# Performance work log

Hardware: AMD Instinct MI355X
Metric: run time of the kernel (lower is better)

The kernel has to match this reference:

```python
import jax, jax.numpy as jnp
import numpy as np

EPS = 1e-5

def layernorm(x, g, b):
    mu = jnp.mean(x, axis=-1, keepdims=True)
    var = jnp.var(x, axis=-1, keepdims=True)
    return (x - mu) / jnp.sqrt(var + EPS) * g + b

def hpmlp(x, wa, ba, wb, bb):
    # Linear(in,H) -> GELU(erf) -> Linear(H,H); dropout is identity in eval
    h = jax.nn.gelu(x @ wa + ba, approximate=False)
    return h @ wb + bb

def setup_inputs() -> dict:
    key = jax.random.key(0)
    ks = jax.random.split(key, 8)
    B, S, H = 16, 4096, 768
    s = 0.02
    return {
        "tokens": jax.random.normal(ks[0], (B, S + 1, H), jnp.float32),
        "lengths": jax.random.randint(ks[1], (B,), 1, S + 1),
        "q": jax.random.normal(ks[2], (2, H), jnp.float32) * s,
        "ln_g": jnp.ones((H,), jnp.float32),
        "ln_b": jnp.zeros((H,), jnp.float32),
        "w1a": jax.random.normal(ks[3], (3 * H, H), jnp.float32) * s,
        "b1a": jnp.zeros((H,), jnp.float32),
        "w1b": jax.random.normal(ks[4], (H, H), jnp.float32) * s,
        "b1b": jnp.zeros((H,), jnp.float32),
        "w2a": jax.random.normal(ks[5], (3 * H, H), jnp.float32) * s,
        "b2a": jnp.zeros((H,), jnp.float32),
        "w2b": jax.random.normal(ks[6], (H, H), jnp.float32) * s,
        "b2b": jnp.zeros((H,), jnp.float32),
    }

def reference(tokens, lengths, q, ln_g, ln_b, w1a, b1a, w1b, b1b, w2a, b2a, w2b, b2b):
    clf = tokens[:, 0]          # [B, H]
    x = tokens[:, 1:]           # [B, S, H]
    B, S, H = x.shape
    mask = jnp.arange(S)[None, :] < lengths[:, None]      # [B, S]
    m3 = mask[..., None]
    denom = lengths.astype(x.dtype)[:, None]
    mean_pooled = jnp.sum(jnp.where(m3, x, 0.0), axis=1) / denom
    max_pooled = jnp.max(jnp.where(m3, x, -jnp.inf), axis=1)
    min_pooled = jnp.min(jnp.where(m3, x, jnp.inf), axis=1)
    # PatchMerger with 2 learned queries over length-masked tokens
    xn = layernorm(x, ln_g, ln_b)                          # [B, S, H]
    logits = jnp.einsum("qh,bsh->bqs", q, xn) * (H ** -0.5)
    logits = jnp.where(mask[:, None, :], logits, -jnp.inf)
    attn = jax.nn.softmax(logits, axis=-1)                 # [B, 2, S]
    pmp = jnp.einsum("bqs,bsh->bqh", attn, xn)             # [B, 2, H]
    pooled_trad = jnp.concatenate([mean_pooled, max_pooled, min_pooled], -1)  # [B, 3H]
    pooled_learn = jnp.concatenate([pmp.reshape(B, 2 * H), clf], -1)          # [B, 3H]
    return jnp.concatenate([
        hpmlp(pooled_trad, w1a, b1a, w1b, b1b),
        hpmlp(pooled_learn, w2a, b2a, w2b, b2b),
    ], -1)
```

## Files before the change

### kernel.cpp

```cpp
#include <hip/hip_runtime.h>
#include <cmath>
#include <cstddef>

#define HD    768
#define BATCH 16
#define SROW  4097
#define NCH   64
#define CS    64
#define TPW   16
#define REC   3856
#define NK1   36
#define NK2   12
#define QSCALE 0.03608439182435161f

__device__ inline void wred4(float& a, float& b, float& c, float& d) {
#pragma unroll
  for (int off = 32; off > 0; off >>= 1) {
    a += __shfl_xor(a, off, 64);
    b += __shfl_xor(b, off, 64);
    c += __shfl_xor(c, off, 64);
    d += __shfl_xor(d, off, 64);
  }
}

__global__ __launch_bounds__(256, 3) void k1_pass(
    const float* __restrict__ tokens, const int* __restrict__ lengths,
    const float* __restrict__ q, const float* __restrict__ ln_g,
    const float* __restrict__ ln_b, float* __restrict__ rec)
{
  const int b = blockIdx.y, c = blockIdx.x;
  const int tid = threadIdx.x, w = tid >> 6, lane = tid & 63;
  const int len = lengths[b];
  if (c * CS >= len) return;

  float gq0[12], gq1[12];
  float G0 = 0.f, G1 = 0.f, C0 = 0.f, C1 = 0.f;
#pragma unroll
  for (int e = 0; e < 3; ++e) {
    const int off = e * 256 + lane * 4;
    const float4 qa = *(const float4*)(q + off);
    const float4 qb = *(const float4*)(q + HD + off);
    const float4 gg = *(const float4*)(ln_g + off);
    const float4 bb = *(const float4*)(ln_b + off);
    const float qav[4] = {qa.x, qa.y, qa.z, qa.w};
    const float qbv[4] = {qb.x, qb.y, qb.z, qb.w};
    const float ggv[4] = {gg.x, gg.y, gg.z, gg.w};
    const float bbv[4] = {bb.x, bb.y, bb.z, bb.w};
#pragma unroll
    for (int j = 0; j < 4; ++j) {
      const float g0 = ggv[j] * qav[j] * QSCALE;
      const float g1 = ggv[j] * qbv[j] * QSCALE;
      gq0[e * 4 + j] = g0;  gq1[e * 4 + j] = g1;
      G0 += g0;  G1 += g1;
      C0 = fmaf(bbv[j] * QSCALE, qav[j], C0);
      C1 = fmaf(bbv[j] * QSCALE, qbv[j], C1);
    }
  }
  wred4(G0, G1, C0, C1);

  float psum[12], pmax[12], pmin[12], A0[12], A1[12];
#pragma unroll
  for (int i = 0; i < 12; ++i) {
    psum[i] = 0.f; pmax[i] = -INFINITY; pmin[i] = INFINITY;
    A0[i] = 0.f; A1[i] = 0.f;
  }
  float m0 = -INFINITY, l0 = 0.f, B0 = 0.f;
  float m1 = -INFINITY, l1 = 0.f, B1 = 0.f;

  const float* xr0 = tokens + ((size_t)b * SROW + 1 + c * CS + w * TPW) * HD
                   + lane * 4;
  const int sbase = c * CS + w * TPW;

  for (int t = 0; t < TPW; ++t) {
    if (sbase + t >= len) break;
    const float* xr = xr0 + (size_t)t * HD;
    float xv[12];
#pragma unroll
    for (int e = 0; e < 3; ++e)
      *(float4*)(xv + 4 * e) = *(const float4*)(xr + e * 256);

    float s1 = 0.f, s2 = 0.f, dx0 = 0.f, dx1 = 0.f;
#pragma unroll
    for (int i = 0; i < 12; ++i) {
      s1 += xv[i];
      s2 = fmaf(xv[i], xv[i], s2);
      dx0 = fmaf(xv[i], gq0[i], dx0);
      dx1 = fmaf(xv[i], gq1[i], dx1);
    }
    wred4(s1, s2, dx0, dx1);
    const float mu   = s1 * (1.f / HD);
    const float var  = fmaf(-mu, mu, s2 * (1.f / HD));
    const float rstd = rsqrtf(var + 1e-5f);
    const float d0 = fmaf(rstd, fmaf(-mu, G0, dx0), C0);
    const float d1 = fmaf(rstd, fmaf(-mu, G1, dx1), C1);

    const float mn0 = fmaxf(m0, d0);
    const float al0 = __expf(m0 - mn0);
    const float p0  = __expf(d0 - mn0);
    const float c0  = p0 * rstd;
    l0 = fmaf(l0, al0, p0);  B0 = fmaf(B0, al0, c0 * mu);  m0 = mn0;

    const float mn1 = fmaxf(m1, d1);
    const float al1 = __expf(m1 - mn1);
    const float p1  = __expf(d1 - mn1);
    const float c1  = p1 * rstd;
    l1 = fmaf(l1, al1, p1);  B1 = fmaf(B1, al1, c1 * mu);  m1 = mn1;

#pragma unroll
    for (int i = 0; i < 12; ++i) {
      psum[i] += xv[i];
      pmax[i] = fmaxf(pmax[i], xv[i]);
      pmin[i] = fminf(pmin[i], xv[i]);
      A0[i] = fmaf(A0[i], al0, c0 * xv[i]);
      A1[i] = fmaf(A1[i], al1, c1 * xv[i]);
    }
  }

  __shared__ float ls[4][2][HD];
  __shared__ float lml[4][6];
#pragma unroll
  for (int e = 0; e < 3; ++e) {
    const int off = e * 256 + lane * 4;
    *(float4*)&ls[w][0][off] = *(const float4*)(psum + 4 * e);
    *(float4*)&ls[w][1][off] = *(const float4*)(pmax + 4 * e);
  }
  if (lane == 0) {
    lml[w][0] = m0; lml[w][1] = l0; lml[w][2] = B0;
    lml[w][3] = m1; lml[w][4] = l1; lml[w][5] = B1;
  }
  __syncthreads();

  float bm0 = -INFINITY, bm1 = -INFINITY;
#pragma unroll
  for (int wv = 0; wv < 4; ++wv) {
    bm0 = fmaxf(bm0, lml[wv][0]);
    bm1 = fmaxf(bm1, lml[wv][3]);
  }
  float sc0[4], sc1[4], bl0 = 0.f, bB0 = 0.f, bl1 = 0.f, bB1 = 0.f;
#pragma unroll
  for (int wv = 0; wv < 4; ++wv) {
    sc0[wv] = (lml[wv][1] > 0.f) ? __expf(lml[wv][0] - bm0) : 0.f;
    sc1[wv] = (lml[wv][4] > 0.f) ? __expf(lml[wv][3] - bm1) : 0.f;
    bl0 = fmaf(lml[wv][1], sc0[wv], bl0);  bB0 = fmaf(lml[wv][2], sc0[wv], bB0);
    bl1 = fmaf(lml[wv][4], sc1[wv], bl1);  bB1 = fmaf(lml[wv][5], sc1[wv], bB1);
  }

  float* r = rec + (size_t)(b * NCH + c) * REC;
#pragma unroll
  for (int e = 0; e < 3; ++e) {
    const int h = tid + 256 * e;
    float su = 0.f, mx = -INFINITY;
#pragma unroll
    for (int wv = 0; wv < 4; ++wv) {
      su += ls[wv][0][h];
      mx = fmaxf(mx, ls[wv][1][h]);
    }
    r[h] = su;  r[HD + h] = mx;
  }
  __syncthreads();
#pragma unroll
  for (int e = 0; e < 3; ++e) {
    const int off = e * 256 + lane * 4;
    *(float4*)&ls[w][0][off] = *(const float4*)(pmin + 4 * e);
    *(float4*)&ls[w][1][off] = *(const float4*)(A0 + 4 * e);
  }
  __syncthreads();
#pragma unroll
  for (int e = 0; e < 3; ++e) {
    const int h = tid + 256 * e;
    float mn_ = INFINITY, a0 = 0.f;
#pragma unroll
    for (int wv = 0; wv < 4; ++wv) {
      mn_ = fminf(mn_, ls[wv][0][h]);
      a0 = fmaf(ls[wv][1][h], sc0[wv], a0);
    }
    r[2 * HD + h] = mn_;  r[3 * HD + h] = a0;
  }
  __syncthreads();
#pragma unroll
  for (int e = 0; e < 3; ++e) {
    const int off = e * 256 + lane * 4;
    *(float4*)&ls[w][0][off] = *(const float4*)(A1 + 4 * e);
  }
  __syncthreads();
#pragma unroll
  for (int e = 0; e < 3; ++e) {
    const int h = tid + 256 * e;
    float a1 = 0.f;
#pragma unroll
    for (int wv = 0; wv < 4; ++wv) a1 = fmaf(ls[wv][0][h], sc1[wv], a1);
    r[4 * HD + h] = a1;
  }
  if (tid == 0) {
    r[3840] = bm0; r[3841] = bl0; r[3842] = bB0;
    r[3843] = bm1; r[3844] = bl1; r[3845] = bB1;
  }
}

__global__ __launch_bounds__(256) void k2_combine(
    const float* __restrict__ rec, const float* __restrict__ tokens,
    const int* __restrict__ lengths, const float* __restrict__ ln_g,
    const float* __restrict__ ln_b, const float* __restrict__ b1b,
    const float* __restrict__ b2b, float* __restrict__ pt,
    float* __restrict__ pl, float* __restrict__ out)
{
  const int b = blockIdx.y, seg = blockIdx.x;
  const int tid = threadIdx.x, ln = tid & 63, cs = tid >> 6;
  const int h = seg * 64 + ln;
  const int len = lengths[b];
  const int nch = (len + CS - 1) / CS;
  const float* rb = rec + (size_t)b * NCH * REC;

  float mg0 = -INFINITY, mg1 = -INFINITY;
  for (int c = 0; c < nch; ++c) {
    const float* rm = rb + (size_t)c * REC + 3840;
    mg0 = fmaxf(mg0, rm[0]);
    mg1 = fmaxf(mg1, rm[3]);
  }
  float lg0 = 0.f, Bg0 = 0.f, lg1 = 0.f, Bg1 = 0.f;
  for (int c = 0; c < nch; ++c) {
    const float* rm = rb + (size_t)c * REC + 3840;
    const float e0 = __expf(rm[0] - mg0);
    const float e1 = __expf(rm[3] - mg1);
    lg0 = fmaf(rm[1], e0, lg0);  Bg0 = fmaf(rm[2], e0, Bg0);
    lg1 = fmaf(rm[4], e1, lg1);  Bg1 = fmaf(rm[5], e1, Bg1);
  }

  float S = 0.f, MX = -INFINITY, MN = INFINITY, A0 = 0.f, A1 = 0.f;
  for (int cc = 0; cc < NCH / 4; ++cc) {
    const int c = cs * (NCH / 4) + cc;
    if (c >= nch) break;
    const float* r = rb + (size_t)c * REC;
    const float e0 = __expf(r[3840] - mg0);
    const float e1 = __expf(r[3843] - mg1);
    S += r[h];
    MX = fmaxf(MX, r[HD + h]);
    MN = fminf(MN, r[2 * HD + h]);
    A0 = fmaf(r[3 * HD + h], e0, A0);
    A1 = fmaf(r[4 * HD + h], e1, A1);
  }

  __shared__ float lbuf[5][4][64];
  lbuf[0][cs][ln] = S;  lbuf[1][cs][ln] = MX; lbuf[2][cs][ln] = MN;
  lbuf[3][cs][ln] = A0; lbuf[4][cs][ln] = A1;
  __syncthreads();
  if (cs == 0) {
#pragma unroll
    for (int k = 1; k < 4; ++k) {
      S  += lbuf[0][k][ln];
      MX  = fmaxf(MX, lbuf[1][k][ln]);
      MN  = fminf(MN, lbuf[2][k][ln]);
      A0 += lbuf[3][k][ln];
      A1 += lbuf[4][k][ln];
    }
    const float invlen = 1.f / (float)len;
    const float il0 = 1.f / lg0, il1 = 1.f / lg1;
    const float gg = ln_g[h], bb = ln_b[h];
    float* ptb = pt + (size_t)b * 2304;
    float* plb = pl + (size_t)b * 2304;
    ptb[h] = S * invlen;
    ptb[HD + h] = MX;
    ptb[2 * HD + h] = MN;
    plb[h]      = fmaf(gg, (A0 - Bg0) * il0, bb);
    plb[HD + h] = fmaf(gg, (A1 - Bg1) * il1, bb);
    plb[2 * HD + h] = tokens[(size_t)b * SROW * HD + h];
  }

  const int gidx = (b * 12 + seg) * 256 + tid;
  if (gidx < 2 * BATCH * HD) {
    const int j = gidx % HD, r2 = (gidx / HD) % 2;
    out[gidx] = (r2 ? b2b : b1b)[j];
  }
}

__global__ __launch_bounds__(256) void k3_gemm1(
    const float* __restrict__ pt, const float* __restrict__ pl,
    const float* __restrict__ w1a, const float* __restrict__ w2a,
    float* __restrict__ part1)
{
  const int kseg = blockIdx.x, jseg = blockIdx.y, mlp = blockIdx.z;
  const int j = jseg * 256 + threadIdx.x;
  const float* xs = mlp ? pl : pt;
  const float* wA = mlp ? w2a : w1a;
  float acc[16];
#pragma unroll
  for (int bb = 0; bb < 16; ++bb) acc[bb] = 0.f;
  const int k0 = kseg * 64;
  for (int kk = 0; kk < 64; ++kk) {
    const int k = k0 + kk;
    const float wv = wA[(size_t)k * HD + j];
#pragma unroll
    for (int bb = 0; bb < 16; ++bb)
      acc[bb] = fmaf(xs[bb * 2304 + k], wv, acc[bb]);
  }
  float* p = part1 + (size_t)(kseg * 2 + mlp) * 16 * HD;
#pragma unroll
  for (int bb = 0; bb < 16; ++bb) p[bb * HD + j] = acc[bb];
}

__global__ __launch_bounds__(256) void k4_gemm2(
    const float* __restrict__ part1, const float* __restrict__ b1a,
    const float* __restrict__ b2a, const float* __restrict__ w1b,
    const float* __restrict__ w2b, float* __restrict__ out)
{
  const int kseg = blockIdx.x, jseg = blockIdx.y, mlp = blockIdx.z;
  const int tid = threadIdx.x;
  const int j = jseg * 256 + tid;
  const int k0 = kseg * 64;
  __shared__ float hs[16][64];

  const float* ba = mlp ? b2a : b1a;
#pragma unroll
  for (int u = 0; u < 4; ++u) {
    const int lin = tid + 256 * u;
    const int bb = lin >> 6, kk = lin & 63;
    const int k = k0 + kk;
    float acc = ba[k];
    for (int ks = 0; ks < NK1; ++ks)
      acc += part1[(size_t)((ks * 2 + mlp) * 16 + bb) * HD + k];
    hs[bb][kk] = 0.5f * acc * (1.f + erff(acc * 0.70710678118654752f));
  }
  __syncthreads();

  const float* wB = mlp ? w2b : w1b;
  float acc2[16];
#pragma unroll
  for (int bb = 0; bb < 16; ++bb) acc2[bb] = 0.f;
  for (int kk = 0; kk < 64; ++kk) {
    const float wv = wB[(size_t)(k0 + kk) * HD + j];
#pragma unroll
    for (int bb = 0; bb < 16; ++bb)
      acc2[bb] = fmaf(hs[bb][kk], wv, acc2[bb]);
  }
#pragma unroll
  for (int bb = 0; bb < 16; ++bb)
    unsafeAtomicAdd(&out[(size_t)bb * 1536 + mlp * HD + j], acc2[bb]);
}

extern "C" void kernel_launch(void* const* d_in, const int* in_sizes, int n_in,
                              void* d_out, int out_size, void* d_ws, size_t ws_size,
                              hipStream_t stream)
{
  const float* tokens = (const float*)d_in[0];
  const int*   lengths = (const int*)d_in[1];
  const float* q    = (const float*)d_in[2];
  const float* ln_g = (const float*)d_in[3];
  const float* ln_b = (const float*)d_in[4];
  const float* w1a  = (const float*)d_in[5];
  const float* b1a  = (const float*)d_in[6];
  const float* w1b  = (const float*)d_in[7];
  const float* b1b  = (const float*)d_in[8];
  const float* w2a  = (const float*)d_in[9];
  const float* b2a  = (const float*)d_in[10];
  const float* w2b  = (const float*)d_in[11];
  const float* b2b  = (const float*)d_in[12];
  float* out = (float*)d_out;

  float* ws    = (float*)d_ws;
  float* rec   = ws;
  float* pt    = rec + (size_t)BATCH * NCH * REC;
  float* pl    = pt + (size_t)BATCH * 2304;
  float* part1 = pl + (size_t)BATCH * 2304;

  hipLaunchKernelGGL(k1_pass, dim3(NCH, BATCH), dim3(256), 0, stream,
                     tokens, lengths, q, ln_g, ln_b, rec);
  hipLaunchKernelGGL(k2_combine, dim3(12, BATCH), dim3(256), 0, stream,
                     rec, tokens, lengths, ln_g, ln_b, b1b, b2b, pt, pl, out);
  hipLaunchKernelGGL(k3_gemm1, dim3(NK1, 3, 2), dim3(256), 0, stream,
                     pt, pl, w1a, w2a, part1);
  hipLaunchKernelGGL(k4_gemm2, dim3(NK2, 3, 2), dim3(256), 0, stream,
                     part1, b1a, b2a, w1b, w2b, out);
}
```

Measured before the change: 359.5 us.

## Prefetch next token row, parallelise softmax stats, atomically reduce GEMM1 partials

The token-streaming loop in k1 now software-prefetches the next row's three float4 loads before working on the current row, so load latency overlaps the reductions. k2 splits the per-chunk max and softmax-normaliser scans across four waves and initialises a hidden buffer with the first-layer biases. k3 halves its K-slice and accumulates into that buffer with atomics instead of writing 72 partial slabs, so k4 no longer sums partials before GELU. This adds atomic contention and register pressure in k1 in exchange for less serial work and less memory traffic.

```diff
diff --git a/kernel.cpp b/kernel.cpp
--- a/kernel.cpp
+++ b/kernel.cpp
@@ -9,8 +9,10 @@
 #define CS    64
 #define TPW   16
 #define REC   3856
-#define NK1   36
-#define NK2   12
+#define NK1   72
+#define K1SEG 32
+#define NK2   24
+#define K2SEG 32
 #define QSCALE 0.03608439182435161f
 
 __device__ inline void wred4(float& a, float& b, float& c, float& d) {
@@ -67,17 +69,30 @@
   float m0 = -INFINITY, l0 = 0.f, B0 = 0.f;
   float m1 = -INFINITY, l1 = 0.f, B1 = 0.f;
 
-  const float* xr0 = tokens + ((size_t)b * SROW + 1 + c * CS + w * TPW) * HD
-                   + lane * 4;
   const int sbase = c * CS + w * TPW;
-
-  for (int t = 0; t < TPW; ++t) {
-    if (sbase + t >= len) break;
-    const float* xr = xr0 + (size_t)t * HD;
+  const int rem0  = len - sbase;
+  const int nt    = rem0 < 0 ? 0 : (rem0 < TPW ? rem0 : TPW);
+
+  const float* xr = tokens + ((size_t)b * SROW + 1 + sbase) * HD + lane * 4;
+
+  float4 nxa, nxb, nxc;
+  if (nt > 0) {
+    nxa = *(const float4*)(xr);
+    nxb = *(const float4*)(xr + 256);
+    nxc = *(const float4*)(xr + 512);
+  }
+
+  for (int t = 0; t < nt; ++t) {
     float xv[12];
-#pragma unroll
-    for (int e = 0; e < 3; ++e)
-      *(float4*)(xv + 4 * e) = *(const float4*)(xr + e * 256);
+    *(float4*)(xv)     = nxa;
+    *(float4*)(xv + 4) = nxb;
+    *(float4*)(xv + 8) = nxc;
+    if (t + 1 < nt) {
+      xr += HD;
+      nxa = *(const float4*)(xr);
+      nxb = *(const float4*)(xr + 256);
+      nxc = *(const float4*)(xr + 512);
+    }
 
     float s1 = 0.f, s2 = 0.f, dx0 = 0.f, dx1 = 0.f;
 #pragma unroll
@@ -200,32 +215,39 @@
 __global__ __launch_bounds__(256) void k2_combine(
     const float* __restrict__ rec, const float* __restrict__ tokens,
     const int* __restrict__ lengths, const float* __restrict__ ln_g,
-    const float* __restrict__ ln_b, const float* __restrict__ b1b,
+    const float* __restrict__ ln_b, const float* __restrict__ b1a,
+    const float* __restrict__ b2a, const float* __restrict__ b1b,
     const float* __restrict__ b2b, float* __restrict__ pt,
-    float* __restrict__ pl, float* __restrict__ out)
+    float* __restrict__ pl, float* __restrict__ hbuf,
+    float* __restrict__ out)
 {
   const int b = blockIdx.y, seg = blockIdx.x;
   const int tid = threadIdx.x, ln = tid & 63, cs = tid >> 6;
-  const int h = seg * 64 + ln;
+  const int h_ = seg * 64 + ln;
   const int len = lengths[b];
   const int nch = (len + CS - 1) / CS;
   const float* rb = rec + (size_t)b * NCH * REC;
 
-  float mg0 = -INFINITY, mg1 = -INFINITY;
-  for (int c = 0; c < nch; ++c) {
+  __shared__ float lmx[4][2];
+  __shared__ float lsc[4][4];
+  __shared__ float lbuf[5][4][64];
+
+  float mq0 = -INFINITY, mq1 = -INFINITY;
+  for (int cc = 0; cc < NCH / 4; ++cc) {
+    const int c = cs * (NCH / 4) + cc;
+    if (c >= nch) break;
     const float* rm = rb + (size_t)c * REC + 3840;
-    mg0 = fmaxf(mg0, rm[0]);
-    mg1 = fmaxf(mg1, rm[3]);
-  }
+    mq0 = fmaxf(mq0, rm[0]);
+    mq1 = fmaxf(mq1, rm[3]);
+  }
+  if (ln == 0) { lmx[cs][0] = mq0; lmx[cs][1] = mq1; }
+  __syncthreads();
+  const float mg0 = fmaxf(fmaxf(lmx[0][0], lmx[1][0]),
+                          fmaxf(lmx[2][0], lmx[3][0]));
+  const float mg1 = fmaxf(fmaxf(lmx[0][1], lmx[1][1]),
+                          fmaxf(lmx[2][1], lmx[3][1]));
+
   float lg0 = 0.f, Bg0 = 0.f, lg1 = 0.f, Bg1 = 0.f;
-  for (int c = 0; c < nch; ++c) {
-    const float* rm = rb + (size_t)c * REC + 3840;
-    const float e0 = __expf(rm[0] - mg0);
-    const float e1 = __expf(rm[3] - mg1);
-    lg0 = fmaf(rm[1], e0, lg0);  Bg0 = fmaf(rm[2], e0, Bg0);
-    lg1 = fmaf(rm[4], e1, lg1);  Bg1 = fmaf(rm[5], e1, Bg1);
-  }
-
   float S = 0.f, MX = -INFINITY, MN = INFINITY, A0 = 0.f, A1 = 0.f;
   for (int cc = 0; cc < NCH / 4; ++cc) {
     const int c = cs * (NCH / 4) + cc;
@@ -233,16 +255,20 @@
     const float* r = rb + (size_t)c * REC;
     const float e0 = __expf(r[3840] - mg0);
     const float e1 = __expf(r[3843] - mg1);
-    S += r[h];
-    MX = fmaxf(MX, r[HD + h]);
-    MN = fminf(MN, r[2 * HD + h]);
-    A0 = fmaf(r[3 * HD + h], e0, A0);
-    A1 = fmaf(r[4 * HD + h], e1, A1);
-  }
-
-  __shared__ float lbuf[5][4][64];
+    lg0 = fmaf(r[3841], e0, lg0);  Bg0 = fmaf(r[3842], e0, Bg0);
+    lg1 = fmaf(r[3844], e1, lg1);  Bg1 = fmaf(r[3845], e1, Bg1);
+    S += r[h_];
+    MX = fmaxf(MX, r[HD + h_]);
+    MN = fminf(MN, r[2 * HD + h_]);
+    A0 = fmaf(r[3 * HD + h_], e0, A0);
+    A1 = fmaf(r[4 * HD + h_], e1, A1);
+  }
+
   lbuf[0][cs][ln] = S;  lbuf[1][cs][ln] = MX; lbuf[2][cs][ln] = MN;
   lbuf[3][cs][ln] = A0; lbuf[4][cs][ln] = A1;
+  if (ln == 0) {
+    lsc[cs][0] = lg0; lsc[cs][1] = Bg0; lsc[cs][2] = lg1; lsc[cs][3] = Bg1;
+  }
   __syncthreads();
   if (cs == 0) {
 #pragma unroll
@@ -253,30 +279,39 @@
       A0 += lbuf[3][k][ln];
       A1 += lbuf[4][k][ln];
     }
+    const float Lg0 = lsc[0][0] + lsc[1][0] + lsc[2][0] + lsc[3][0];
+    const float BG0 = lsc[0][1] + lsc[1][1] + lsc[2][1] + lsc[3][1];
+    const float Lg1 = lsc[0][2] + lsc[1][2] + lsc[2][2] + lsc[3][2];
+    const float BG1 = lsc[0][3] + lsc[1][3] + lsc[2][3] + lsc[3][3];
     const float invlen = 1.f / (float)len;
-    const float il0 = 1.f / lg0, il1 = 1.f / lg1;
-    const float gg = ln_g[h], bb = ln_b[h];
+    const float il0 = 1.f / Lg0, il1 = 1.f / Lg1;
+    const float gg = ln_g[h_], bb = ln_b[h_];
     float* ptb = pt + (size_t)b * 2304;
     float* plb = pl + (size_t)b * 2304;
-    ptb[h] = S * invlen;
-    ptb[HD + h] = MX;
-    ptb[2 * HD + h] = MN;
-    plb[h]      = fmaf(gg, (A0 - Bg0) * il0, bb);
-    plb[HD + h] = fmaf(gg, (A1 - Bg1) * il1, bb);
-    plb[2 * HD + h] = tokens[(size_t)b * SROW * HD + h];
+    ptb[h_] = S * invlen;
+    ptb[HD + h_] = MX;
+    ptb[2 * HD + h_] = MN;
+    plb[h_]      = fmaf(gg, (A0 - BG0) * il0, bb);
+    plb[HD + h_] = fmaf(gg, (A1 - BG1) * il1, bb);
+    plb[2 * HD + h_] = tokens[(size_t)b * SROW * HD + h_];
   }
 
   const int gidx = (b * 12 + seg) * 256 + tid;
   if (gidx < 2 * BATCH * HD) {
-    const int j = gidx % HD, r2 = (gidx / HD) % 2;
+    const int j = gidx % HD, r2 = (gidx / HD) & 1;
     out[gidx] = (r2 ? b2b : b1b)[j];
+  } else {
+    const int g2 = gidx - 2 * BATCH * HD;
+    const int j = g2 % HD;
+    const int mlp = g2 / (BATCH * HD);
+    hbuf[g2] = (mlp ? b2a : b1a)[j];
   }
 }
 
 __global__ __launch_bounds__(256) void k3_gemm1(
     const float* __restrict__ pt, const float* __restrict__ pl,
     const float* __restrict__ w1a, const float* __restrict__ w2a,
-    float* __restrict__ part1)
+    float* __restrict__ hbuf)
 {
   const int kseg = blockIdx.x, jseg = blockIdx.y, mlp = blockIdx.z;
   const int j = jseg * 256 + threadIdx.x;
@@ -285,40 +320,38 @@
   float acc[16];
 #pragma unroll
   for (int bb = 0; bb < 16; ++bb) acc[bb] = 0.f;
-  const int k0 = kseg * 64;
-  for (int kk = 0; kk < 64; ++kk) {
+  const int k0 = kseg * K1SEG;
+#pragma unroll 4
+  for (int kk = 0; kk < K1SEG; ++kk) {
     const int k = k0 + kk;
     const float wv = wA[(size_t)k * HD + j];
 #pragma unroll
     for (int bb = 0; bb < 16; ++bb)
       acc[bb] = fmaf(xs[bb * 2304 + k], wv, acc[bb]);
   }
-  float* p = part1 + (size_t)(kseg * 2 + mlp) * 16 * HD;
-#pragma unroll
-  for (int bb = 0; bb < 16; ++bb) p[bb * HD + j] = acc[bb];
+  float* hm = hbuf + (size_t)mlp * BATCH * HD;
+#pragma unroll
+  for (int bb = 0; bb < 16; ++bb)
+    unsafeAtomicAdd(&hm[bb * HD + j], acc[bb]);
 }
 
 __global__ __launch_bounds__(256) void k4_gemm2(
-    const float* __restrict__ part1, const float* __restrict__ b1a,
-    const float* __restrict__ b2a, const float* __restrict__ w1b,
+    const float* __restrict__ hbuf, const float* __restrict__ w1b,
     const float* __restrict__ w2b, float* __restrict__ out)
 {
   const int kseg = blockIdx.x, jseg = blockIdx.y, mlp = blockIdx.z;
   const int tid = threadIdx.x;
   const int j = jseg * 256 + tid;
-  const int k0 = kseg * 64;
-  __shared__ float hs[16][64];
-
-  const float* ba = mlp ? b2a : b1a;
-#pragma unroll
-  for (int u = 0; u < 4; ++u) {
+  const int k0 = kseg * K2SEG;
+  __shared__ float hs[16][K2SEG];
+
+  const float* hm = hbuf + (size_t)mlp * BATCH * HD;
+#pragma unroll
+  for (int u = 0; u < (16 * K2SEG) / 256; ++u) {
     const int lin = tid + 256 * u;
-    const int bb = lin >> 6, kk = lin & 63;
-    const int k = k0 + kk;
-    float acc = ba[k];
-    for (int ks = 0; ks < NK1; ++ks)
-      acc += part1[(size_t)((ks * 2 + mlp) * 16 + bb) * HD + k];
-    hs[bb][kk] = 0.5f * acc * (1.f + erff(acc * 0.70710678118654752f));
+    const int bb = lin / K2SEG, kk = lin % K2SEG;
+    const float a = hm[bb * HD + k0 + kk];
+    hs[bb][kk] = 0.5f * a * (1.f + erff(a * 0.70710678118654752f));
   }
   __syncthreads();
 
@@ -326,7 +359,8 @@
   float acc2[16];
 #pragma unroll
   for (int bb = 0; bb < 16; ++bb) acc2[bb] = 0.f;
-  for (int kk = 0; kk < 64; ++kk) {
+#pragma unroll 4
+  for (int kk = 0; kk < K2SEG; ++kk) {
     const float wv = wB[(size_t)(k0 + kk) * HD + j];
 #pragma unroll
     for (int bb = 0; bb < 16; ++bb)
@@ -356,18 +390,19 @@
   const float* b2b  = (const float*)d_in[12];
   float* out = (float*)d_out;
 
-  float* ws    = (float*)d_ws;
-  float* rec   = ws;
-  float* pt    = rec + (size_t)BATCH * NCH * REC;
-  float* pl    = pt + (size_t)BATCH * 2304;
-  float* part1 = pl + (size_t)BATCH * 2304;
+  float* ws   = (float*)d_ws;
+  float* rec  = ws;
+  float* pt   = rec + (size_t)BATCH * NCH * REC;
+  float* pl   = pt + (size_t)BATCH * 2304;
+  float* hbuf = pl + (size_t)BATCH * 2304;
 
   hipLaunchKernelGGL(k1_pass, dim3(NCH, BATCH), dim3(256), 0, stream,
                      tokens, lengths, q, ln_g, ln_b, rec);
   hipLaunchKernelGGL(k2_combine, dim3(12, BATCH), dim3(256), 0, stream,
-                     rec, tokens, lengths, ln_g, ln_b, b1b, b2b, pt, pl, out);
+                     rec, tokens, lengths, ln_g, ln_b, b1a, b2a, b1b, b2b,
+                     pt, pl, hbuf, out);
   hipLaunchKernelGGL(k3_gemm1, dim3(NK1, 3, 2), dim3(256), 0, stream,
-                     pt, pl, w1a, w2a, part1);
+                     pt, pl, w1a, w2a, hbuf);
   hipLaunchKernelGGL(k4_gemm2, dim3(NK2, 3, 2), dim3(256), 0, stream,
-                     part1, b1a, b2a, w1b, w2b, out);
-}
+                     hbuf, w1b, w2b, out);
+}
```

After: 310.0 us. -13.8%, faster.
